# Kernel tuning notes

Measured on AMD Instinct MI355X. Metric: run time of the kernel, lower is better.

## Reference

```python
import jax, jax.numpy as jnp
import numpy as np

NL, B, L, D, V = 8, 8, 2048, 768, 50288
HALT_ID = 50277
EPS = 1e-5


def setup_inputs() -> dict:
    key = jax.random.key(0)
    ks = jax.random.split(key, 6)
    x_steps = jax.random.normal(ks[0], (NL, B, L, D), jnp.float32)
    residual_steps = jax.random.normal(ks[1], (NL, B, L, D), jnp.float32)
    norm_weight = jnp.ones((D,), jnp.float32)
    lm_head_weight = jax.random.normal(ks[2], (V, D), jnp.float32) * 0.02
    ans_starts = jax.random.randint(ks[3], (B,), 1, L)            # valid answer positions
    chain_lens = jax.random.randint(ks[4], (B,), 1, NL + 1)       # ragged chain lengths
    chain_targets = jax.random.randint(ks[5], (B, NL), 0, V)
    # last target of each chain is <HALT> (as in training data)
    chain_targets = chain_targets.at[jnp.arange(B), chain_lens - 1].set(HALT_ID)
    return {
        "x_steps": x_steps,
        "residual_steps": residual_steps,
        "norm_weight": norm_weight,
        "lm_head_weight": lm_head_weight,
        "ans_starts": ans_starts,
        "chain_targets": chain_targets,
        "chain_lens": chain_lens,
    }


def _forward(x_steps, residual_steps, norm_weight, lm_head_weight,
             ans_starts, chain_targets, chain_lens):
    n_loops, Bn, Ln, Dn = x_steps.shape
    Vn = lm_head_weight.shape[0]
    b_idx = jnp.arange(Bn)

    # gather the single answer position per batch (logits_step[b, as_-1, :])
    pos = jnp.clip(ans_starts - 1, 0, Ln - 1)                     # [B]
    xg = x_steps[:, b_idx, pos]                                   # [NL,B,D]
    rg = residual_steps[:, b_idx, pos]                            # [NL,B,D]

    # norm_f(x, residual, prenorm=False) == RMSNorm(x + residual)
    h = xg + rg
    h = h * jax.lax.rsqrt(jnp.mean(h * h, axis=-1, keepdims=True) + EPS) * norm_weight

    # lm_head on the gathered positions only (same math as full logits + gather)
    logits = jnp.einsum("lbd,vd->lbv", h, lm_head_weight)         # [NL,B,V]

    # target id: btgt[min(loop_i, len(btgt)-1)]
    loop_i = jnp.arange(n_loops)[:, None]                         # [NL,1]
    tidx = jnp.minimum(loop_i, chain_lens[None, :] - 1)           # [NL,B]
    tgt = chain_targets[b_idx[None, :], tidx]                     # [NL,B]

    valid = (ans_starts[None, :] >= 1) & (ans_starts[None, :] < Ln) & (tgt < Vn)
    vf = valid.astype(jnp.float32)

    # full-vocab cross entropy per (loop, batch)
    logZ = jax.scipy.special.logsumexp(logits, axis=-1)           # [NL,B]
    tgt_logit = jnp.take_along_axis(logits, tgt[..., None], axis=-1)[..., 0]
    ce = logZ - tgt_logit                                         # [NL,B]

    pred = jnp.argmax(logits, axis=-1)                            # [NL,B]
    correct = (pred == tgt).astype(jnp.float32)

    cnt = vf.sum(axis=1)                                          # valid per loop
    has = cnt > 0
    hasf = has.astype(jnp.float32)
    denom = jnp.maximum(cnt, 1.0)
    loop_loss = jnp.where(has, (ce * vf).sum(axis=1) / denom, 0.0)
    loop_acc = jnp.where(has, (correct * vf).sum(axis=1) / denom, 0.0)

    n_has = hasf.sum()
    avg_loss = (loop_loss * hasf).sum() / jnp.maximum(n_has, 1.0)
    avg_acc = (loop_acc * hasf).sum() / jnp.maximum(n_has, 1.0)

    # answer_acc = mean of step_accs[:-1] (drop last valid loop) if >1 valid loop
    last_valid = n_loops - 1 - jnp.argmax(has[::-1])
    drop_last = hasf * (jnp.arange(n_loops) != last_valid).astype(jnp.float32)
    ans_mask = jnp.where(n_has > 1, drop_last, hasf)
    answer_acc = jnp.where(ans_mask.sum() > 0,
                           (loop_acc * ans_mask).sum() / jnp.maximum(ans_mask.sum(), 1.0),
                           avg_acc)

    hm = vf * (tgt == HALT_ID).astype(jnp.float32)
    halt_acc = jnp.where(hm.sum() > 0,
                         (correct * hm).sum() / jnp.maximum(hm.sum(), 1.0),
                         0.0)
    return avg_loss, avg_acc, answer_acc, halt_acc


def reference(x_steps, residual_steps, norm_weight, lm_head_weight,
              ans_starts, chain_targets, chain_lens):
    return _forward(x_steps, residual_steps, norm_weight, lm_head_weight,
                    ans_starts, chain_targets, chain_lens)
```

## Files before the change

kernel.cpp:

```cpp
#include <hip/hip_runtime.h>
#include <hip/hip_bf16.h>
#include <math.h>

#define NLOOP 8
#define BB 8
#define LLEN 2048
#define DD 768
#define VV 50288
#define HALT 50277
#define EPSF 1e-5f

#define BN 64
#define BKK 32
#define KSTEPS (DD / BKK)
#define NBLK ((VV + BN - 1) / BN)
#define PFD 6

typedef short bf16x8 __attribute__((ext_vector_type(8)));
typedef float f32x4 __attribute__((ext_vector_type(4)));

#define LGKM_BARRIER() asm volatile("s_waitcnt lgkmcnt(0)\n\ts_barrier" ::: "memory")

__device__ __forceinline__ unsigned short f32_to_bf16(float f) {
    unsigned u = __builtin_bit_cast(unsigned, f);
    unsigned r = (u + 0x7FFFu + ((u >> 16) & 1u)) >> 16;
    return (unsigned short)r;
}

__global__ __launch_bounds__(256) void k_prep(
    const float* __restrict__ x, const float* __restrict__ res,
    const float* __restrict__ nw, const float* __restrict__ W,
    const int* __restrict__ ans_starts, const int* __restrict__ chain_targets,
    const int* __restrict__ chain_lens,
    unsigned short* __restrict__ hbf, float* __restrict__ tgt_logit,
    unsigned int* __restrict__ counter)
{
    if (blockIdx.x == 0 && threadIdx.x == 0) *counter = 0u;

    int lb = blockIdx.x, l = lb >> 3, b = lb & 7;
    int tid = threadIdx.x, lane = tid & 63, wave = tid >> 6;
    int as = ans_starts[b];
    int pos = as - 1;
    pos = pos < 0 ? 0 : (pos > LLEN - 1 ? LLEN - 1 : pos);
    size_t base = ((size_t)lb * LLEN + (size_t)pos) * DD;

    float hv[3];
    float ss = 0.f;
#pragma unroll
    for (int i = 0; i < 3; ++i) {
        int d = tid + i * 256;
        float v = x[base + d] + res[base + d];
        hv[i] = v;
        ss += v * v;
    }
#pragma unroll
    for (int off = 32; off; off >>= 1) ss += __shfl_down(ss, off);
    __shared__ float red[4];
    __shared__ float bc;
    if (lane == 0) red[wave] = ss;
    __syncthreads();
    if (tid == 0) bc = red[0] + red[1] + red[2] + red[3];
    __syncthreads();
    float rs = rsqrtf(bc / (float)DD + EPSF);

    int cl = chain_lens[b];
    int tix = l < cl - 1 ? l : cl - 1;
    int tgt = chain_targets[b * NLOOP + tix];
    bool tok = (tgt >= 0) && (tgt < VV);

    float dp = 0.f;
#pragma unroll
    for (int i = 0; i < 3; ++i) {
        int d = tid + i * 256;
        float h = hv[i] * rs * nw[d];
        hbf[(size_t)lb * DD + d] = f32_to_bf16(h);
        if (tok) dp += h * W[(size_t)tgt * DD + d];
    }
#pragma unroll
    for (int off = 32; off; off >>= 1) dp += __shfl_down(dp, off);
    __syncthreads();
    if (lane == 0) red[wave] = dp;
    __syncthreads();
    if (tid == 0) tgt_logit[lb] = red[0] + red[1] + red[2] + red[3];
}

__global__ __launch_bounds__(256, 2) void k_logits(
    const float* __restrict__ W, const unsigned short* __restrict__ hbf,
    float* __restrict__ pmax, float* __restrict__ psum, int* __restrict__ parg)
{
    __shared__ unsigned short Bs[2][64 * 56];

    int blk = blockIdx.x;
    int v0 = blk * BN;
    int tid = threadIdx.x;
    int wave = tid >> 6, lane = tid & 63, q = lane >> 4, c = lane & 15;

    const unsigned short* Ap = hbf + (size_t)(16 * wave + c) * DD + q * 8;
    bf16x8 A[KSTEPS];
#pragma unroll
    for (int ks = 0; ks < KSTEPS; ++ks)
        A[ks] = *(const bf16x8*)(Ap + ks * BKK);

    int r1 = tid >> 3, koff = (tid & 7) * 4;
    int vB0 = v0 + r1, vB1 = v0 + r1 + 32;
    const float* gB0 = W + (size_t)(vB0 < VV ? vB0 : 0) * DD + koff;
    const float* gB1 = W + (size_t)(vB1 < VV ? vB1 : 0) * DD + koff;

    f32x4 acc[4];
#pragma unroll
    for (int n = 0; n < 4; ++n) acc[n] = (f32x4){0.f, 0.f, 0.f, 0.f};

    auto stage_write = [&](int bufi, const f32x4& ra, const f32x4& rb) {
        ushort4 w0, w1;
        w0.x = f32_to_bf16(ra[0]); w0.y = f32_to_bf16(ra[1]);
        w0.z = f32_to_bf16(ra[2]); w0.w = f32_to_bf16(ra[3]);
        w1.x = f32_to_bf16(rb[0]); w1.y = f32_to_bf16(rb[1]);
        w1.z = f32_to_bf16(rb[2]); w1.w = f32_to_bf16(rb[3]);
        *(ushort4*)&Bs[bufi][r1 * 56 + koff] = w0;
        *(ushort4*)&Bs[bufi][(r1 + 32) * 56 + koff] = w1;
    };
    auto mfma_step = [&](int bufi, int ks) {
        bf16x8 f0 = *(const bf16x8*)&Bs[bufi][(c +  0) * 56 + q * 8];
        bf16x8 f1 = *(const bf16x8*)&Bs[bufi][(c + 16) * 56 + q * 8];
        bf16x8 f2 = *(const bf16x8*)&Bs[bufi][(c + 32) * 56 + q * 8];
        bf16x8 f3 = *(const bf16x8*)&Bs[bufi][(c + 48) * 56 + q * 8];
        acc[0] = __builtin_amdgcn_mfma_f32_16x16x32_bf16(A[ks], f0, acc[0], 0, 0, 0);
        acc[1] = __builtin_amdgcn_mfma_f32_16x16x32_bf16(A[ks], f1, acc[1], 0, 0, 0);
        acc[2] = __builtin_amdgcn_mfma_f32_16x16x32_bf16(A[ks], f2, acc[2], 0, 0, 0);
        acc[3] = __builtin_amdgcn_mfma_f32_16x16x32_bf16(A[ks], f3, acc[3], 0, 0, 0);
    };

    f32x4 pa[PFD], pb[PFD];
#pragma unroll
    for (int i = 0; i < PFD; ++i) {
        pa[i] = __builtin_nontemporal_load((const f32x4*)(gB0 + i * BKK));
        pb[i] = __builtin_nontemporal_load((const f32x4*)(gB1 + i * BKK));
    }

#pragma unroll
    for (int ks = 0; ks < KSTEPS; ++ks) {
        const int slot = ks % PFD;
        const int bufi = ks & 1;
        stage_write(bufi, pa[slot], pb[slot]);
        LGKM_BARRIER();
        if (ks + PFD < KSTEPS) {
            pa[slot] = __builtin_nontemporal_load((const f32x4*)(gB0 + (ks + PFD) * BKK));
            pb[slot] = __builtin_nontemporal_load((const f32x4*)(gB1 + (ks + PFD) * BKK));
        }
        mfma_step(bufi, ks);
    }

    const float NEGINF = -__builtin_inff();
#pragma unroll
    for (int r = 0; r < 4; ++r) {
        float val = NEGINF; int idx = 0x7fffffff;
#pragma unroll
        for (int n = 0; n < 4; ++n) {
            int colg = v0 + 16 * n + c;
            float v = (colg < VV) ? acc[n][r] : NEGINF;
            if (v > val || (v == val && colg < idx)) { val = v; idx = colg; }
        }
#pragma unroll
        for (int off = 1; off < 16; off <<= 1) {
            float ov = __shfl_xor(val, off);
            int oi = __shfl_xor(idx, off);
            if (ov > val || (ov == val && oi < idx)) { val = ov; idx = oi; }
        }
        float M = val;
        float e = 0.f;
#pragma unroll
        for (int n = 0; n < 4; ++n) {
            int colg = v0 + 16 * n + c;
            e += (colg < VV) ? __expf(acc[n][r] - M) : 0.f;
        }
#pragma unroll
        for (int off = 1; off < 16; off <<= 1) e += __shfl_xor(e, off);
        if (c == 0) {
            int row = 16 * wave + 4 * q + r;
            pmax[(size_t)row * NBLK + blk] = M;
            psum[(size_t)row * NBLK + blk] = e;
            parg[(size_t)row * NBLK + blk] = idx;
        }
    }
}

__global__ __launch_bounds__(256) void k_combine(
    const float* __restrict__ pmax, const float* __restrict__ psum,
    const int* __restrict__ parg, const float* __restrict__ tgt_logit,
    const int* __restrict__ ans_starts, const int* __restrict__ chain_targets,
    const int* __restrict__ chain_lens,
    float* __restrict__ logZ, int* __restrict__ pred,
    unsigned int* __restrict__ counter, float* __restrict__ out)
{
    int r = blockIdx.x;
    int tid = threadIdx.x;
    int wave = tid >> 6, lane = tid & 63;
    const float NEGINF = -__builtin_inff();

    const float* pm = pmax + (size_t)r * NBLK;
    const float* ps = psum + (size_t)r * NBLK;
    const int*   pa = parg + (size_t)r * NBLK;

    float M = NEGINF; int A_ = 0x7fffffff;
    for (int i = tid; i < NBLK; i += 256) {
        float m = pm[i];
        int a = pa[i];
        if (m > M || (m == M && a < A_)) { M = m; A_ = a; }
    }
#pragma unroll
    for (int off = 1; off < 64; off <<= 1) {
        float ov = __shfl_xor(M, off);
        int oa = __shfl_xor(A_, off);
        if (ov > M || (ov == M && oa < A_)) { M = ov; A_ = oa; }
    }
    __shared__ float sm[4]; __shared__ int sa[4]; __shared__ float ssum[4];
    __shared__ int lastflag;
    if (lane == 0) { sm[wave] = M; sa[wave] = A_; }
    __syncthreads();
    if (tid == 0) {
#pragma unroll
        for (int w = 1; w < 4; ++w)
            if (sm[w] > sm[0] || (sm[w] == sm[0] && sa[w] < sa[0])) { sm[0] = sm[w]; sa[0] = sa[w]; }
    }
    __syncthreads();
    float Mg = sm[0];

    float S = 0.f;
    for (int i = tid; i < NBLK; i += 256)
        S += ps[i] * __expf(pm[i] - Mg);
#pragma unroll
    for (int off = 1; off < 64; off <<= 1) S += __shfl_xor(S, off);
    if (lane == 0) ssum[wave] = S;
    __syncthreads();
    if (tid == 0) {
        float lz = Mg + logf(ssum[0] + ssum[1] + ssum[2] + ssum[3]);
        __hip_atomic_store(&logZ[r], lz, __ATOMIC_RELAXED, __HIP_MEMORY_SCOPE_AGENT);
        __hip_atomic_store(&pred[r], sa[0], __ATOMIC_RELAXED, __HIP_MEMORY_SCOPE_AGENT);
        __threadfence();
        unsigned int old = atomicAdd(counter, 1u);
        lastflag = (old == 63u) ? 1 : 0;
    }
    __syncthreads();
    if (lastflag == 0) return;

    __threadfence();
    __shared__ float lzs[64]; __shared__ int prs[64];
    if (tid < 64) {
        lzs[tid] = __hip_atomic_load(&logZ[tid], __ATOMIC_RELAXED, __HIP_MEMORY_SCOPE_AGENT);
        prs[tid] = __hip_atomic_load(&pred[tid], __ATOMIC_RELAXED, __HIP_MEMORY_SCOPE_AGENT);
    }
    __syncthreads();
    if (tid == 0) {
        float loop_loss[NLOOP], loop_acc[NLOOP], hasf[NLOOP];
        float n_has = 0.f, hms = 0.f, hcs = 0.f;
        for (int l = 0; l < NLOOP; ++l) {
            float cnt = 0.f, se = 0.f, sc = 0.f;
            for (int b = 0; b < BB; ++b) {
                int cl = chain_lens[b];
                int ti = l < cl - 1 ? l : cl - 1;
                int tgt = chain_targets[b * NLOOP + ti];
                int as = ans_starts[b];
                bool valid = (as >= 1) && (as < LLEN) && (tgt < VV);
                int idx = l * BB + b;
                float ce = lzs[idx] - tgt_logit[idx];
                float corr = (prs[idx] == tgt) ? 1.f : 0.f;
                if (valid) {
                    cnt += 1.f; se += ce; sc += corr;
                    if (tgt == HALT) { hms += 1.f; hcs += corr; }
                }
            }
            bool has = cnt > 0.f;
            hasf[l] = has ? 1.f : 0.f;
            n_has += hasf[l];
            float denom = cnt > 1.f ? cnt : 1.f;
            loop_loss[l] = has ? se / denom : 0.f;
            loop_acc[l]  = has ? sc / denom : 0.f;
        }
        float nn = n_has > 1.f ? n_has : 1.f;
        float avg_loss = 0.f, avg_acc = 0.f;
        for (int l = 0; l < NLOOP; ++l) {
            avg_loss += loop_loss[l] * hasf[l];
            avg_acc  += loop_acc[l]  * hasf[l];
        }
        avg_loss /= nn; avg_acc /= nn;
        int last_valid = NLOOP - 1;
        for (int l = NLOOP - 1; l >= 0; --l) if (hasf[l] > 0.f) { last_valid = l; break; }
        float ams = 0.f, aacc = 0.f;
        for (int l = 0; l < NLOOP; ++l) {
            float mask = (n_has > 1.f) ? (hasf[l] * ((l != last_valid) ? 1.f : 0.f)) : hasf[l];
            ams += mask; aacc += loop_acc[l] * mask;
        }
        float answer_acc = (ams > 0.f) ? (aacc / (ams > 1.f ? ams : 1.f)) : avg_acc;
        float halt_acc = (hms > 0.f) ? (hcs / (hms > 1.f ? hms : 1.f)) : 0.f;
        out[0] = avg_loss; out[1] = avg_acc; out[2] = answer_acc; out[3] = halt_acc;
    }
}

extern "C" void kernel_launch(void* const* d_in, const int* in_sizes, int n_in,
                              void* d_out, int out_size, void* d_ws, size_t ws_size,
                              hipStream_t stream) {
    const float* x   = (const float*)d_in[0];
    const float* res = (const float*)d_in[1];
    const float* nw  = (const float*)d_in[2];
    const float* W   = (const float*)d_in[3];
    const int* ans   = (const int*)d_in[4];
    const int* ct    = (const int*)d_in[5];
    const int* cl    = (const int*)d_in[6];
    float* out = (float*)d_out;

    char* ws = (char*)d_ws;
    unsigned short* hbf = (unsigned short*)ws;
    float* tgtl = (float*)(ws + 98304);
    size_t off = 98560;
    float* pmax = (float*)(ws + off);  off += (size_t)64 * NBLK * 4;
    float* psum = (float*)(ws + off);  off += (size_t)64 * NBLK * 4;
    int*   parg = (int*)  (ws + off);  off += (size_t)64 * NBLK * 4;
    float* logZ = (float*)(ws + off);  off += 256;
    int*   pred = (int*)  (ws + off);  off += 256;
    unsigned int* counter = (unsigned int*)(ws + off); off += 256;

    k_prep<<<64, 256, 0, stream>>>(x, res, nw, W, ans, ct, cl, hbf, tgtl, counter);
    k_logits<<<NBLK, 256, 0, stream>>>(W, hbf, pmax, psum, parg);
    k_combine<<<64, 256, 0, stream>>>(pmax, psum, parg, tgtl, ans, ct, cl,
                                      logZ, pred, counter, out);
}
```

Baseline: 59.82 us.

## Use XOR-swizzled unpadded LDS tile with 8-wide per-thread weight rows

Changes the weight staging so each thread loads 8 contiguous floats from one row instead of 4 floats from each of two rows. Each thread then writes a single 16-byte bf16 vector into an unpadded 32-wide LDS tile, with an XOR swizzle that replaces the padding as the bank-conflict fix. It also cuts the prefetch depth from 6 to 4, drops the occupancy hint in launch bounds, and switches nontemporal loads to plain loads. The aims are fewer LDS instructions, a smaller LDS footprint and lower register pressure. The shallower prefetch may expose more memory latency.

After: 58.32 us. 1.03x faster.

```diff
diff --git a/kernel.cpp b/kernel.cpp
--- a/kernel.cpp
+++ b/kernel.cpp
@@ -14,7 +14,7 @@
 #define BKK 32
 #define KSTEPS (DD / BKK)
 #define NBLK ((VV + BN - 1) / BN)
-#define PFD 6
+#define PFD 4
 
 typedef short bf16x8 __attribute__((ext_vector_type(8)));
 typedef float f32x4 __attribute__((ext_vector_type(4)));
@@ -84,11 +84,11 @@
     if (tid == 0) tgt_logit[lb] = red[0] + red[1] + red[2] + red[3];
 }
 
-__global__ __launch_bounds__(256, 2) void k_logits(
+__global__ __launch_bounds__(256) void k_logits(
     const float* __restrict__ W, const unsigned short* __restrict__ hbf,
     float* __restrict__ pmax, float* __restrict__ psum, int* __restrict__ parg)
 {
-    __shared__ unsigned short Bs[2][64 * 56];
+    __shared__ unsigned short Bs[2][64 * 32];
 
     int blk = blockIdx.x;
     int v0 = blk * BN;
@@ -101,29 +101,30 @@
     for (int ks = 0; ks < KSTEPS; ++ks)
         A[ks] = *(const bf16x8*)(Ap + ks * BKK);
 
-    int r1 = tid >> 3, koff = (tid & 7) * 4;
-    int vB0 = v0 + r1, vB1 = v0 + r1 + 32;
-    const float* gB0 = W + (size_t)(vB0 < VV ? vB0 : 0) * DD + koff;
-    const float* gB1 = W + (size_t)(vB1 < VV ? vB1 : 0) * DD + koff;
+    int r1 = tid >> 2, j2 = tid & 3;
+    int vB = v0 + r1;
+    const float* gB = W + (size_t)(vB < VV ? vB : 0) * DD + j2 * 8;
 
     f32x4 acc[4];
 #pragma unroll
     for (int n = 0; n < 4; ++n) acc[n] = (f32x4){0.f, 0.f, 0.f, 0.f};
 
+    const int uw = (j2 ^ ((r1 >> 1) & 3)) * 8;
+    const int ur = (q ^ ((c >> 1) & 3)) * 8;
+
     auto stage_write = [&](int bufi, const f32x4& ra, const f32x4& rb) {
-        ushort4 w0, w1;
-        w0.x = f32_to_bf16(ra[0]); w0.y = f32_to_bf16(ra[1]);
-        w0.z = f32_to_bf16(ra[2]); w0.w = f32_to_bf16(ra[3]);
-        w1.x = f32_to_bf16(rb[0]); w1.y = f32_to_bf16(rb[1]);
-        w1.z = f32_to_bf16(rb[2]); w1.w = f32_to_bf16(rb[3]);
-        *(ushort4*)&Bs[bufi][r1 * 56 + koff] = w0;
-        *(ushort4*)&Bs[bufi][(r1 + 32) * 56 + koff] = w1;
+        bf16x8 v;
+        v[0] = (short)f32_to_bf16(ra[0]); v[1] = (short)f32_to_bf16(ra[1]);
+        v[2] = (short)f32_to_bf16(ra[2]); v[3] = (short)f32_to_bf16(ra[3]);
+        v[4] = (short)f32_to_bf16(rb[0]); v[5] = (short)f32_to_bf16(rb[1]);
+        v[6] = (short)f32_to_bf16(rb[2]); v[7] = (short)f32_to_bf16(rb[3]);
+        *(bf16x8*)&Bs[bufi][r1 * 32 + uw] = v;
     };
     auto mfma_step = [&](int bufi, int ks) {
-        bf16x8 f0 = *(const bf16x8*)&Bs[bufi][(c +  0) * 56 + q * 8];
-        bf16x8 f1 = *(const bf16x8*)&Bs[bufi][(c + 16) * 56 + q * 8];
-        bf16x8 f2 = *(const bf16x8*)&Bs[bufi][(c + 32) * 56 + q * 8];
-        bf16x8 f3 = *(const bf16x8*)&Bs[bufi][(c + 48) * 56 + q * 8];
+        bf16x8 f0 = *(const bf16x8*)&Bs[bufi][(c +  0) * 32 + ur];
+        bf16x8 f1 = *(const bf16x8*)&Bs[bufi][(c + 16) * 32 + ur];
+        bf16x8 f2 = *(const bf16x8*)&Bs[bufi][(c + 32) * 32 + ur];
+        bf16x8 f3 = *(const bf16x8*)&Bs[bufi][(c + 48) * 32 + ur];
         acc[0] = __builtin_amdgcn_mfma_f32_16x16x32_bf16(A[ks], f0, acc[0], 0, 0, 0);
         acc[1] = __builtin_amdgcn_mfma_f32_16x16x32_bf16(A[ks], f1, acc[1], 0, 0, 0);
         acc[2] = __builtin_amdgcn_mfma_f32_16x16x32_bf16(A[ks], f2, acc[2], 0, 0, 0);
@@ -133,8 +134,8 @@
     f32x4 pa[PFD], pb[PFD];
 #pragma unroll
     for (int i = 0; i < PFD; ++i) {
-        pa[i] = __builtin_nontemporal_load((const f32x4*)(gB0 + i * BKK));
-        pb[i] = __builtin_nontemporal_load((const f32x4*)(gB1 + i * BKK));
+        pa[i] = *(const f32x4*)(gB + i * BKK);
+        pb[i] = *(const f32x4*)(gB + i * BKK + 4);
     }
 
 #pragma unroll
@@ -144,8 +145,8 @@
         stage_write(bufi, pa[slot], pb[slot]);
         LGKM_BARRIER();
         if (ks + PFD < KSTEPS) {
-            pa[slot] = __builtin_nontemporal_load((const f32x4*)(gB0 + (ks + PFD) * BKK));
-            pb[slot] = __builtin_nontemporal_load((const f32x4*)(gB1 + (ks + PFD) * BKK));
+            pa[slot] = *(const f32x4*)(gB + (ks + PFD) * BKK);
+            pb[slot] = *(const f32x4*)(gB + (ks + PFD) * BKK + 4);
         }
         mfma_step(bufi, ks);
     }
```
